# Performance work log

Measured on AMD Instinct MI355X. Metric: run time of the kernel, lower is better.

Reference implementation:

```python
import jax, jax.numpy as jnp
import numpy as np

DVEC = 128
B, S = 4, 1024


def setup_inputs() -> dict:
    key = jax.random.key(0)
    k1, k2 = jax.random.split(key)
    func_and_arg = jax.random.normal(k1, (B, S, 2 * DVEC), dtype=jnp.float32)
    cooccurrences = jax.random.normal(k2, (DVEC, DVEC, DVEC), dtype=jnp.float32)
    return {"func_and_arg": func_and_arg, "cooccurrences": cooccurrences}


def reference(func_and_arg, cooccurrences):
    # out[b,s,z] = sum_{i,j} func[b,s,i] * cooc[i,j,z] * arg[b,s,j]
    d = cooccurrences.shape[0]
    func = func_and_arg[..., :d]   # [B,S,D]
    arg = func_and_arg[..., d:]    # [B,S,D]
    # contract func over i first -> [B,S,D(j),Z], then arg over j -> [B,S,Z]
    tmp = jnp.einsum('bsi,ijz->bsjz', func, cooccurrences)
    return jnp.einsum('bsjz,bsj->bsz', tmp, arg)
```

## Files before the change

### kernel.cpp

```cpp
#include <hip/hip_runtime.h>
#include <hip/hip_bf16.h>


typedef __attribute__((ext_vector_type(8))) short bf16x8;
typedef __attribute__((ext_vector_type(4))) float f32x4;

__device__ __forceinline__ unsigned pkbf16(float x, float y) {
    __hip_bfloat162 h = __float22bfloat162_rn(make_float2(x, y));
    unsigned u; __builtin_memcpy(&u, &h, sizeof(u));
    return u;
}

__global__ __launch_bounds__(256) void cooc_transpose(
    const float* __restrict__ Cc, ushort* __restrict__ CT)
{
    __shared__ float tile[32][132];
    const int i  = blockIdx.x >> 2;
    const int j0 = (blockIdx.x & 3) * 32;
    const int t  = threadIdx.x;
    {
        const int jj = t >> 3;
        const int zb = (t & 7) * 16;
        const float* src = Cc + (size_t)i * 16384 + (size_t)(j0 + jj) * 128 + zb;
        #pragma unroll
        for (int k = 0; k < 4; ++k)
            *(float4*)&tile[jj][zb + k * 4] = *(const float4*)(src + k * 4);
    }
    __syncthreads();
    {
        const int z = t >> 1;
        const int h = t & 1;
        unsigned o[8];
        #pragma unroll
        for (int p = 0; p < 8; ++p)
            o[p] = pkbf16(tile[h * 16 + 2 * p][z], tile[h * 16 + 2 * p + 1][z]);
        ushort* dst = CT + (size_t)i * 16384 + (size_t)z * 128 + j0 + h * 16;
        *(uint4*)dst       = make_uint4(o[0], o[1], o[2], o[3]);
        *(uint4*)(dst + 8) = make_uint4(o[4], o[5], o[6], o[7]);
    }
}

template<int USE_WS>
__global__ __launch_bounds__(256, 2) void cooc_main(
    const float* __restrict__ fa, const ushort* __restrict__ CT,
    float* __restrict__ dst)
{
    __shared__ float f_lds[16][128];

    const int bid = blockIdx.x;
    const int kp = bid & 7, zp = (bid >> 3) & 1, mtile = bid >> 4;
    const int t0 = mtile * 128, i0 = kp * 16, z0 = zp * 64;
    const int tid = threadIdx.x, lane = tid & 63, wv = tid >> 6;
    const int lm = lane & 15, lk = lane >> 4;

    {
        const int row = tid & 127;
        const int sh = (tid >> 7) * 8;
        const float* fp = fa + (size_t)(t0 + row) * 256 + i0 + sh;
        float4 v0 = *(const float4*)fp;
        float4 v1 = *(const float4*)(fp + 4);
        f_lds[sh + 0][row] = v0.x; f_lds[sh + 1][row] = v0.y;
        f_lds[sh + 2][row] = v0.z; f_lds[sh + 3][row] = v0.w;
        f_lds[sh + 4][row] = v1.x; f_lds[sh + 5][row] = v1.y;
        f_lds[sh + 6][row] = v1.z; f_lds[sh + 7][row] = v1.w;
    }

    union { unsigned u[4]; bf16x8 v; } a_pk[8][4];
    #pragma unroll
    for (int m = 0; m < 8; ++m) {
        const float* ab = fa + (size_t)(t0 + m * 16 + lm) * 256 + 128;
        #pragma unroll
        for (int ks = 0; ks < 4; ++ks) {
            float4 q0 = *(const float4*)(ab + ks * 32 + lk * 8);
            float4 q1 = *(const float4*)(ab + ks * 32 + lk * 8 + 4);
            a_pk[m][ks].u[0] = pkbf16(q0.x, q0.y);
            a_pk[m][ks].u[1] = pkbf16(q0.z, q0.w);
            a_pk[m][ks].u[2] = pkbf16(q1.x, q1.y);
            a_pk[m][ks].u[3] = pkbf16(q1.z, q1.w);
        }
    }
    __syncthreads();

    const ushort* bsrc = CT + (size_t)i0 * 16384
                            + (size_t)(z0 + wv * 16 + lm) * 128 + lk * 8;

    bf16x8 B[2][4];
    #pragma unroll
    for (int ks = 0; ks < 4; ++ks)
        B[0][ks] = *(const bf16x8*)(bsrc + ks * 32);

    float acc[8][4];
    #pragma unroll
    for (int m = 0; m < 8; ++m)
        #pragma unroll
        for (int r = 0; r < 4; ++r) acc[m][r] = 0.f;

    #pragma unroll 2
    for (int s = 0; s < 16; ++s) {
        const int cur = s & 1;
        if (s < 15) {
            const ushort* p = bsrc + (size_t)(s + 1) * 16384;
            #pragma unroll
            for (int ks = 0; ks < 4; ++ks)
                B[cur ^ 1][ks] = *(const bf16x8*)(p + ks * 32);
        }
        #pragma unroll
        for (int h = 0; h < 2; ++h) {
            float4 f4[4];
            #pragma unroll
            for (int mm = 0; mm < 4; ++mm)
                f4[mm] = *(const float4*)&f_lds[s][(h * 4 + mm) * 16 + lk * 4];

            f32x4 g[4];
            #pragma unroll
            for (int mm = 0; mm < 4; ++mm) g[mm] = (f32x4){0.f, 0.f, 0.f, 0.f};

            #pragma unroll
            for (int ks = 0; ks < 4; ++ks)
                #pragma unroll
                for (int mm = 0; mm < 4; ++mm)
                    g[mm] = __builtin_amdgcn_mfma_f32_16x16x32_bf16(
                        a_pk[h * 4 + mm][ks].v, B[cur][ks], g[mm], 0, 0, 0);

            #pragma unroll
            for (int mm = 0; mm < 4; ++mm) {
                acc[h * 4 + mm][0] += f4[mm].x * g[mm][0];
                acc[h * 4 + mm][1] += f4[mm].y * g[mm][1];
                acc[h * 4 + mm][2] += f4[mm].z * g[mm][2];
                acc[h * 4 + mm][3] += f4[mm].w * g[mm][3];
            }
        }
    }

    const int col = z0 + wv * 16 + lm;
    #pragma unroll
    for (int m = 0; m < 8; ++m)
        #pragma unroll
        for (int r = 0; r < 4; ++r) {
            const int row = t0 + m * 16 + lk * 4 + r;
            if (USE_WS)
                dst[(size_t)kp * 524288 + (size_t)row * 128 + col] = acc[m][r];
            else
                atomicAdd(&dst[(size_t)row * 128 + col], acc[m][r]);
        }
}

__global__ __launch_bounds__(256) void cooc_reduce(const float* __restrict__ ws,
                                                   float* __restrict__ out) {
    const size_t idx = ((size_t)blockIdx.x * 256 + threadIdx.x) * 4;
    float4 a = *(const float4*)(ws + idx);
    #pragma unroll
    for (int k = 1; k < 8; ++k) {
        float4 b = *(const float4*)(ws + (size_t)k * 524288 + idx);
        a.x += b.x; a.y += b.y; a.z += b.z; a.w += b.w;
    }
    *(float4*)(out + idx) = a;
}

extern "C" void kernel_launch(void* const* d_in, const int* in_sizes, int n_in,
                              void* d_out, int out_size, void* d_ws, size_t ws_size,
                              hipStream_t stream) {
    const float* fa = (const float*)d_in[0];
    const float* Cc = (const float*)d_in[1];
    float* out = (float*)d_out;

    const size_t PART = (size_t)8 * 524288;
    const size_t CTOF = PART * sizeof(float);
    const size_t NEED_FULL = CTOF + (size_t)128 * 128 * 128 * 2;
    const size_t NEED_CT   = (size_t)128 * 128 * 128 * 2;

    if (ws_size >= NEED_FULL) {
        ushort* CT = (ushort*)((char*)d_ws + CTOF);
        cooc_transpose<<<512, 256, 0, stream>>>(Cc, CT);
        cooc_main<1><<<512, 256, 0, stream>>>(fa, CT, (float*)d_ws);
        cooc_reduce<<<512, 256, 0, stream>>>((const float*)d_ws, out);
    } else if (ws_size >= NEED_CT) {
        ushort* CT = (ushort*)d_ws;
        cooc_transpose<<<512, 256, 0, stream>>>(Cc, CT);
        (void)hipMemsetAsync(out, 0, (size_t)out_size * sizeof(float), stream);
        cooc_main<0><<<512, 256, 0, stream>>>(fa, CT, out);
    } else {
        (void)hipMemsetAsync(out, 0, (size_t)out_size * sizeof(float), stream);
        cooc_main<0><<<512, 256, 0, stream>>>(fa, (const ushort*)d_ws, out);
    }
}
```

Before: 102.6 us.

## Pre-pack arg operand to bf16 and store cooc in MFMA-fragment layout

Adds a small kernel that converts the arg half of the inputs to bf16 once and stores it in the per-lane MFMA fragment order. Each main-kernel block then loads its A fragments with contiguous 16-byte loads instead of converting fp32 strided data; previously this was redone by every one of the 16 blocks sharing a row tile. The transposed cooc tensor is also written in fragment-contiguous order so B loads within a wave are fully coalesced. The cost is an extra kernel launch, additional workspace, and one more pass over the arg data.

Result: faster. 89.03 us (-13.3%).

```diff
diff --git a/kernel.cpp b/kernel.cpp
--- a/kernel.cpp
+++ b/kernel.cpp
@@ -34,16 +34,32 @@
         #pragma unroll
         for (int p = 0; p < 8; ++p)
             o[p] = pkbf16(tile[h * 16 + 2 * p][z], tile[h * 16 + 2 * p + 1][z]);
-        ushort* dst = CT + (size_t)i * 16384 + (size_t)z * 128 + j0 + h * 16;
-        *(uint4*)dst       = make_uint4(o[0], o[1], o[2], o[3]);
-        *(uint4*)(dst + 8) = make_uint4(o[4], o[5], o[6], o[7]);
-    }
+        const int c0 = (j0 >> 3) + h * 2;
+        ushort* dst = CT + (size_t)i * 16384 + (size_t)(z >> 4) * 2048
+                         + (size_t)c0 * 128 + (z & 15) * 8;
+        *(uint4*)dst         = make_uint4(o[0], o[1], o[2], o[3]);
+        *(uint4*)(dst + 128) = make_uint4(o[4], o[5], o[6], o[7]);
+    }
+}
+
+__global__ __launch_bounds__(256) void cooc_apack(
+    const float* __restrict__ fa, ushort* __restrict__ APK)
+{
+    const int g = blockIdx.x;
+    const int t = threadIdx.x;
+    const int ks = t >> 6, lk = (t >> 4) & 3, lm = t & 15;
+    const float* src = fa + (size_t)(g * 16 + lm) * 256 + 128 + ks * 32 + lk * 8;
+    float4 q0 = *(const float4*)src;
+    float4 q1 = *(const float4*)(src + 4);
+    unsigned o0 = pkbf16(q0.x, q0.y), o1 = pkbf16(q0.z, q0.w);
+    unsigned o2 = pkbf16(q1.x, q1.y), o3 = pkbf16(q1.z, q1.w);
+    *(uint4*)(APK + (size_t)g * 2048 + t * 8) = make_uint4(o0, o1, o2, o3);
 }
 
 template<int USE_WS>
 __global__ __launch_bounds__(256, 2) void cooc_main(
     const float* __restrict__ fa, const ushort* __restrict__ CT,
-    float* __restrict__ dst)
+    const ushort* __restrict__ APK, float* __restrict__ dst)
 {
     __shared__ float f_lds[16][128];
 
@@ -65,29 +81,24 @@
         f_lds[sh + 6][row] = v1.z; f_lds[sh + 7][row] = v1.w;
     }
 
-    union { unsigned u[4]; bf16x8 v; } a_pk[8][4];
-    #pragma unroll
-    for (int m = 0; m < 8; ++m) {
-        const float* ab = fa + (size_t)(t0 + m * 16 + lm) * 256 + 128;
-        #pragma unroll
-        for (int ks = 0; ks < 4; ++ks) {
-            float4 q0 = *(const float4*)(ab + ks * 32 + lk * 8);
-            float4 q1 = *(const float4*)(ab + ks * 32 + lk * 8 + 4);
-            a_pk[m][ks].u[0] = pkbf16(q0.x, q0.y);
-            a_pk[m][ks].u[1] = pkbf16(q0.z, q0.w);
-            a_pk[m][ks].u[2] = pkbf16(q1.x, q1.y);
-            a_pk[m][ks].u[3] = pkbf16(q1.z, q1.w);
-        }
+    bf16x8 a_pk[8][4];
+    {
+        const ushort* ap = APK + (size_t)(t0 >> 4) * 2048 + lane * 8;
+        #pragma unroll
+        for (int m = 0; m < 8; ++m)
+            #pragma unroll
+            for (int ks = 0; ks < 4; ++ks)
+                a_pk[m][ks] = *(const bf16x8*)(ap + (size_t)m * 2048 + ks * 512);
     }
     __syncthreads();
 
     const ushort* bsrc = CT + (size_t)i0 * 16384
-                            + (size_t)(z0 + wv * 16 + lm) * 128 + lk * 8;
+                            + (size_t)(zp * 4 + wv) * 2048 + lane * 8;
 
     bf16x8 B[2][4];
     #pragma unroll
     for (int ks = 0; ks < 4; ++ks)
-        B[0][ks] = *(const bf16x8*)(bsrc + ks * 32);
+        B[0][ks] = *(const bf16x8*)(bsrc + ks * 512);
 
     float acc[8][4];
     #pragma unroll
@@ -102,7 +113,7 @@
             const ushort* p = bsrc + (size_t)(s + 1) * 16384;
             #pragma unroll
             for (int ks = 0; ks < 4; ++ks)
-                B[cur ^ 1][ks] = *(const bf16x8*)(p + ks * 32);
+                B[cur ^ 1][ks] = *(const bf16x8*)(p + ks * 512);
         }
         #pragma unroll
         for (int h = 0; h < 2; ++h) {
@@ -120,7 +131,7 @@
                 #pragma unroll
                 for (int mm = 0; mm < 4; ++mm)
                     g[mm] = __builtin_amdgcn_mfma_f32_16x16x32_bf16(
-                        a_pk[h * 4 + mm][ks].v, B[cur][ks], g[mm], 0, 0, 0);
+                        a_pk[h * 4 + mm][ks], B[cur][ks], g[mm], 0, 0, 0);
 
             #pragma unroll
             for (int mm = 0; mm < 4; ++mm) {
@@ -166,21 +177,29 @@
 
     const size_t PART = (size_t)8 * 524288;
     const size_t CTOF = PART * sizeof(float);
-    const size_t NEED_FULL = CTOF + (size_t)128 * 128 * 128 * 2;
-    const size_t NEED_CT   = (size_t)128 * 128 * 128 * 2;
+    const size_t CTSZ = (size_t)128 * 128 * 128 * 2;
+    const size_t APOF = CTOF + CTSZ;
+    const size_t APSZ = (size_t)4096 * 128 * 2;
+    const size_t NEED_FULL = APOF + APSZ;
+    const size_t NEED_CT   = CTSZ + APSZ;
 
     if (ws_size >= NEED_FULL) {
-        ushort* CT = (ushort*)((char*)d_ws + CTOF);
+        ushort* CT  = (ushort*)((char*)d_ws + CTOF);
+        ushort* APK = (ushort*)((char*)d_ws + APOF);
         cooc_transpose<<<512, 256, 0, stream>>>(Cc, CT);
-        cooc_main<1><<<512, 256, 0, stream>>>(fa, CT, (float*)d_ws);
+        cooc_apack<<<256, 256, 0, stream>>>(fa, APK);
+        cooc_main<1><<<512, 256, 0, stream>>>(fa, CT, APK, (float*)d_ws);
         cooc_reduce<<<512, 256, 0, stream>>>((const float*)d_ws, out);
     } else if (ws_size >= NEED_CT) {
-        ushort* CT = (ushort*)d_ws;
+        ushort* CT  = (ushort*)d_ws;
+        ushort* APK = (ushort*)((char*)d_ws + CTSZ);
         cooc_transpose<<<512, 256, 0, stream>>>(Cc, CT);
+        cooc_apack<<<256, 256, 0, stream>>>(fa, APK);
         (void)hipMemsetAsync(out, 0, (size_t)out_size * sizeof(float), stream);
-        cooc_main<0><<<512, 256, 0, stream>>>(fa, CT, out);
+        cooc_main<0><<<512, 256, 0, stream>>>(fa, CT, APK, out);
     } else {
         (void)hipMemsetAsync(out, 0, (size_t)out_size * sizeof(float), stream);
-        cooc_main<0><<<512, 256, 0, stream>>>(fa, (const ushort*)d_ws, out);
-    }
-}
+        cooc_main<0><<<512, 256, 0, stream>>>(fa, (const ushort*)d_ws,
+                                              (const ushort*)d_ws, out);
+    }
+}
```
